# Kernel tuning notes

Hardware: AMD Instinct MI355X
Metric: run time of the kernel (lower is better)

Reference implementation:

```python
import jax, jax.numpy as jnp
import numpy as np

BATCH = 65536
FEAT_DIM = 512
NUM_CLASS = 16
LAMDA = 1.0
LAMDA1 = 10.0
SCALE = 1.0
EPS = 1e-9


def setup_inputs() -> dict:
    key = jax.random.key(0)
    k1, k2, k3 = jax.random.split(key, 3)
    output_features = jax.random.normal(k1, (BATCH, FEAT_DIM), dtype=jnp.float32)
    y_truth = jax.random.randint(k2, (BATCH,), 0, NUM_CLASS, dtype=jnp.int64)
    feature_centers = jax.random.normal(k3, (NUM_CLASS, FEAT_DIM), dtype=jnp.float32)
    return {
        "output_features": output_features,
        "y_truth": y_truth,
        "feature_centers": feature_centers,
    }


def reference(output_features, y_truth, feature_centers):
    batch_size = output_features.shape[0]
    factor = SCALE / batch_size

    # Center loss: gather per-sample class center, squared diff, sum.
    centers_batch = feature_centers[y_truth]              # [B, D]
    diff = output_features - centers_batch
    loss_center = 0.5 * jnp.sum(diff * diff) * factor

    # Pairwise cosine similarity over class centers (upper triangle, j<k),
    # replacing the O(C^2) python loop with one matmul + mask + reduce.
    norms = jnp.sqrt(jnp.sum(feature_centers * feature_centers, axis=1))  # [C]
    gram = feature_centers @ feature_centers.T                            # [C, C]
    denom = norms[:, None] * norms[None, :] + EPS
    cos = gram / denom
    c = feature_centers.shape[0]
    upper = jnp.triu(jnp.ones((c, c), dtype=bool), k=1)
    item1_sum = jnp.sum(jnp.where(upper, cos + 1.0, 0.0))

    loss_island = LAMDA * (loss_center + LAMDA1 * item1_sum)
    return loss_island
```

## Files before the change

kernel.cpp:

```cpp
#include <hip/hip_runtime.h>
#include <math.h>

#define BATCH    65536
#define FEAT     512
#define NCLASS   16
#define LAMDA    1.0f
#define LAMDA1   10.0f
#define SCALE    1.0f
#define EPS      1e-9f

constexpr int BLOCK  = 256;
constexpr int GRID   = 4096;
constexpr int NV     = BATCH * (FEAT / 4);
constexpr int STRIDE = GRID * BLOCK;
constexpr int ITERS  = NV / STRIDE;

__global__ __launch_bounds__(BLOCK) void center_loss_kernel(
    const float4* __restrict__ x,
    const int*    __restrict__ y,
    const float4* __restrict__ centers4,
    float*        __restrict__ accum)
{
    __shared__ float4 cl[NCLASS * (FEAT / 4)];
    __shared__ float  wsum[4];

    const int tid = blockIdx.x * BLOCK + threadIdx.x;
    const int base_b = __builtin_amdgcn_readfirstlane(tid >> 7);
    const int d4     = tid & 127;

    #pragma unroll
    for (int k = 0; k < 8; ++k)
        cl[threadIdx.x + k * BLOCK] = centers4[threadIdx.x + k * BLOCK];

    int cls[ITERS];
    #pragma unroll
    for (int it = 0; it < ITERS; ++it)
        cls[it] = y[base_b + it * (STRIDE >> 7)];

    __syncthreads();

    float sum = 0.0f;
    #pragma unroll
    for (int it = 0; it < ITERS; ++it) {
        float4 xv = x[tid + it * STRIDE];
        float4 cv = cl[cls[it] * (FEAT / 4) + d4];
        float e0 = xv.x - cv.x;
        float e1 = xv.y - cv.y;
        float e2 = xv.z - cv.z;
        float e3 = xv.w - cv.w;
        sum += e0 * e0 + e1 * e1 + e2 * e2 + e3 * e3;
    }

    #pragma unroll
    for (int off = 32; off > 0; off >>= 1)
        sum += __shfl_down(sum, off, 64);

    const int lane = threadIdx.x & 63;
    const int wid  = threadIdx.x >> 6;
    if (lane == 0) wsum[wid] = sum;
    __syncthreads();
    if (threadIdx.x == 0) {
        atomicAdd(accum, wsum[0] + wsum[1] + wsum[2] + wsum[3]);
    }
}

__global__ __launch_bounds__(256) void finalize_kernel(
    const float4* __restrict__ centers4,
    const float*  __restrict__ accum,
    float*        __restrict__ out)
{
    __shared__ float gram[NCLASS][NCLASS];
    const int j = threadIdx.x >> 4;
    const int k = threadIdx.x & 15;
    const float4* cj = centers4 + j * (FEAT / 4);
    const float4* ck = centers4 + k * (FEAT / 4);
    float dot = 0.0f;
    #pragma unroll 8
    for (int i = 0; i < FEAT / 4; ++i) {
        float4 a = cj[i];
        float4 b = ck[i];
        dot += a.x * b.x + a.y * b.y + a.z * b.z + a.w * b.w;
    }
    gram[j][k] = dot;
    __syncthreads();

    if (threadIdx.x == 0) {
        float item1 = 0.0f;
        for (int jj = 0; jj < NCLASS; ++jj) {
            float nj = sqrtf(gram[jj][jj]);
            for (int kk = jj + 1; kk < NCLASS; ++kk) {
                float nk = sqrtf(gram[kk][kk]);
                item1 += gram[jj][kk] / (nj * nk + EPS) + 1.0f;
            }
        }
        float loss_center = 0.5f * accum[0] * (SCALE / (float)BATCH);
        out[0] = LAMDA * (loss_center + LAMDA1 * item1);
    }
}

extern "C" void kernel_launch(void* const* d_in, const int* in_sizes, int n_in,
                              void* d_out, int out_size, void* d_ws, size_t ws_size,
                              hipStream_t stream) {
    const float* x       = (const float*)d_in[0];
    const int*   y       = (const int*)d_in[1];
    const float* centers = (const float*)d_in[2];
    float* out   = (float*)d_out;
    float* accum = (float*)d_ws;

    hipMemsetAsync(accum, 0, sizeof(float), stream);

    center_loss_kernel<<<GRID, BLOCK, 0, stream>>>(
        (const float4*)x, y, (const float4*)centers, accum);

    finalize_kernel<<<1, 256, 0, stream>>>((const float4*)centers, accum, out);
}
```

Baseline: 234.9 us.

## Read centers from global memory and replace atomic with per-block partials

Drops the per-block staging of all 16 class centers (32KB) into shared memory and the barrier that follows it; the gathered center rows are now read directly from global memory, relying on cache hits since the table is small. The single global atomicAdd is replaced by per-block partial sums written to workspace and reduced in the finalize kernel, which also removes the memset launch. This trades redundant staging work and LDS occupancy pressure for cached global gathers.

After: 214.8 us. 1.09x faster.

```diff
diff --git a/kernel.cpp b/kernel.cpp
--- a/kernel.cpp
+++ b/kernel.cpp
@@ -19,31 +19,23 @@
     const float4* __restrict__ x,
     const int*    __restrict__ y,
     const float4* __restrict__ centers4,
-    float*        __restrict__ accum)
+    float*        __restrict__ partials)
 {
-    __shared__ float4 cl[NCLASS * (FEAT / 4)];
-    __shared__ float  wsum[4];
+    const int tid = blockIdx.x * BLOCK + threadIdx.x;
 
-    const int tid = blockIdx.x * BLOCK + threadIdx.x;
     const int base_b = __builtin_amdgcn_readfirstlane(tid >> 7);
     const int d4     = tid & 127;
-
-    #pragma unroll
-    for (int k = 0; k < 8; ++k)
-        cl[threadIdx.x + k * BLOCK] = centers4[threadIdx.x + k * BLOCK];
 
     int cls[ITERS];
     #pragma unroll
     for (int it = 0; it < ITERS; ++it)
         cls[it] = y[base_b + it * (STRIDE >> 7)];
 
-    __syncthreads();
-
     float sum = 0.0f;
     #pragma unroll
     for (int it = 0; it < ITERS; ++it) {
         float4 xv = x[tid + it * STRIDE];
-        float4 cv = cl[cls[it] * (FEAT / 4) + d4];
+        float4 cv = centers4[cls[it] * (FEAT / 4) + d4];
         float e0 = xv.x - cv.x;
         float e1 = xv.y - cv.y;
         float e2 = xv.z - cv.z;
@@ -55,20 +47,34 @@
     for (int off = 32; off > 0; off >>= 1)
         sum += __shfl_down(sum, off, 64);
 
+    __shared__ float wsum[4];
     const int lane = threadIdx.x & 63;
     const int wid  = threadIdx.x >> 6;
     if (lane == 0) wsum[wid] = sum;
     __syncthreads();
     if (threadIdx.x == 0) {
-        atomicAdd(accum, wsum[0] + wsum[1] + wsum[2] + wsum[3]);
+        partials[blockIdx.x] = wsum[0] + wsum[1] + wsum[2] + wsum[3];
     }
 }
 
 __global__ __launch_bounds__(256) void finalize_kernel(
     const float4* __restrict__ centers4,
-    const float*  __restrict__ accum,
+    const float*  __restrict__ partials,
     float*        __restrict__ out)
 {
+    float psum = 0.0f;
+    #pragma unroll
+    for (int k = 0; k < GRID / 256; ++k)
+        psum += partials[threadIdx.x + k * 256];
+    #pragma unroll
+    for (int off = 32; off > 0; off >>= 1)
+        psum += __shfl_down(psum, off, 64);
+
+    __shared__ float wsum[4];
+    const int lane = threadIdx.x & 63;
+    const int wid  = threadIdx.x >> 6;
+    if (lane == 0) wsum[wid] = psum;
+
     __shared__ float gram[NCLASS][NCLASS];
     const int j = threadIdx.x >> 4;
     const int k = threadIdx.x & 15;
@@ -93,7 +99,8 @@
                 item1 += gram[jj][kk] / (nj * nk + EPS) + 1.0f;
             }
         }
-        float loss_center = 0.5f * accum[0] * (SCALE / (float)BATCH);
+        float total = wsum[0] + wsum[1] + wsum[2] + wsum[3];
+        float loss_center = 0.5f * total * (SCALE / (float)BATCH);
         out[0] = LAMDA * (loss_center + LAMDA1 * item1);
     }
 }
@@ -101,16 +108,14 @@
 extern "C" void kernel_launch(void* const* d_in, const int* in_sizes, int n_in,
                               void* d_out, int out_size, void* d_ws, size_t ws_size,
                               hipStream_t stream) {
-    const float* x       = (const float*)d_in[0];
-    const int*   y       = (const int*)d_in[1];
-    const float* centers = (const float*)d_in[2];
-    float* out   = (float*)d_out;
-    float* accum = (float*)d_ws;
-
-    hipMemsetAsync(accum, 0, sizeof(float), stream);
+    const float* x        = (const float*)d_in[0];
+    const int*   y        = (const int*)d_in[1];
+    const float* centers  = (const float*)d_in[2];
+    float* out      = (float*)d_out;
+    float* partials = (float*)d_ws;
 
     center_loss_kernel<<<GRID, BLOCK, 0, stream>>>(
-        (const float4*)x, y, (const float4*)centers, accum);
+        (const float4*)x, y, (const float4*)centers, partials);
 
-    finalize_kernel<<<1, 256, 0, stream>>>((const float4*)centers, accum, out);
+    finalize_kernel<<<1, 256, 0, stream>>>((const float4*)centers, partials, out);
 }
```
